# Kernel tuning notes

Measured on AMD Instinct MI355X. Metric: run time of the kernel, lower is better.

Reference implementation:

```python
import jax, jax.numpy as jnp
import numpy as np

BLOCK_SIZE = 32
QMAX = 31.0   # 6-bit symmetric: representable range [-32, 31], scale by absmax/31
QMIN = -32.0


def axs6_dequant(w: jnp.ndarray, block_size: int = BLOCK_SIZE) -> jnp.ndarray:
    """Block-wise 6-bit symmetric fake-quantization (quantize + dequantize)."""
    shape = w.shape
    wf = w.reshape(-1, block_size)                       # [n_blocks, block]
    scale = jnp.max(jnp.abs(wf), axis=1, keepdims=True) / QMAX
    scale = jnp.where(scale == 0, jnp.ones_like(scale), scale)
    q = jnp.clip(jnp.round(wf / scale), QMIN, QMAX)
    return (q * scale).reshape(shape)


def setup_inputs() -> dict:
    key = jax.random.key(0)
    k_x, k_w, k_b = jax.random.split(key, 3)
    C_in, C_out, K = 256, 512, 3
    x = jax.random.normal(k_x, (32, C_in, 56, 56), dtype=jnp.float32)
    # kaiming_uniform_(a=sqrt(5)) -> bound = sqrt(6 / ((1 + 5) * fan_in)) = 1/sqrt(fan_in)
    fan_in = C_in * K * K
    bound = 1.0 / np.sqrt(fan_in)
    weight = jax.random.uniform(k_w, (C_out, C_in, K, K), dtype=jnp.float32,
                                minval=-bound, maxval=bound)
    bias = jax.random.uniform(k_b, (C_out,), dtype=jnp.float32,
                              minval=-bound, maxval=bound)
    return {"x": x, "weight": weight, "bias": bias}


def reference(x, weight, bias):
    w_dq = axs6_dequant(weight, BLOCK_SIZE)
    out = jax.lax.conv_general_dilated(
        x, w_dq,
        window_strides=(1, 1),
        padding=((1, 1), (1, 1)),
        rhs_dilation=(1, 1),
        feature_group_count=1,
        dimension_numbers=("NCHW", "OIHW", "NCHW"),
    )
    return out + bias[None, :, None, None]
```

## Files before the change

kernel.cpp:

```cpp
#include <hip/hip_runtime.h>
#include <hip/hip_bf16.h>

typedef __bf16 bf16_t;
typedef __attribute__((ext_vector_type(8))) __bf16 bf16x8;
typedef __attribute__((ext_vector_type(4))) float f32x4;
typedef __attribute__((ext_vector_type(4))) int   i32x4;

#define C_IN   256
#define C_OUT  512
#define HW     3136
#define NB     32
#define HP     58
#define NQBLK  36864

#define NT   36
#define NWG  896

typedef const __attribute__((address_space(1))) unsigned int gu32;
typedef __attribute__((address_space(3))) unsigned int lu32;
__device__ __forceinline__ void gl16(const void* g, void* l) {
    __builtin_amdgcn_global_load_lds((gu32*)g, (lu32*)l, 16, 0, 0);
}
#define BAR()    __builtin_amdgcn_s_barrier()
#define PRIO(x)  __builtin_amdgcn_s_setprio(x)
#define SCHED0() __builtin_amdgcn_sched_barrier(0)

__device__ __forceinline__ bf16x8 asbf(i32x4 v) {
    union { i32x4 a; bf16x8 b; } u; u.a = v; return u.b;
}
__device__ __forceinline__ f32x4 MF(i32x4 a, i32x4 b, f32x4 c) {
    return __builtin_amdgcn_mfma_f32_16x16x32_bf16(asbf(a), asbf(b), c, 0, 0, 0);
}

__global__ void k_dequant(const float* __restrict__ w, bf16_t* __restrict__ wt) {
    int b = blockIdx.x * blockDim.x + threadIdx.x;
    if (b >= NQBLK) return;
    const float* src = w + (size_t)b * 32;
    float v[32];
    float amax = 0.f;
    #pragma unroll
    for (int i = 0; i < 32; i += 4) {
        float4 t = *reinterpret_cast<const float4*>(src + i);
        v[i] = t.x; v[i+1] = t.y; v[i+2] = t.z; v[i+3] = t.w;
        amax = fmaxf(amax, fmaxf(fmaxf(fabsf(t.x), fabsf(t.y)),
                                 fmaxf(fabsf(t.z), fabsf(t.w))));
    }
    float scale = amax / 31.0f;
    if (scale == 0.f) scale = 1.f;
    #pragma unroll
    for (int i = 0; i < 32; i++) {
        float q = rintf(v[i] / scale);
        q = fminf(31.f, fmaxf(-32.f, q));
        float dq = q * scale;
        int flat = b * 32 + i;
        int p    = flat % 9;
        int rest = flat / 9;
        int ci   = rest & 255;
        int co   = rest >> 8;
        wt[((size_t)(p * C_OUT + co) << 8) + ci] = (bf16_t)dq;
    }
}

__global__ void k_halo_zero(bf16_t* __restrict__ xT) {
    int idx = blockIdx.x * 256 + threadIdx.x;
    if (idx >= NB * 228 * 32) return;
    int c8 = idx & 31;
    int t  = idx >> 5;
    int p  = t % 228;
    int n  = t / 228;
    int hh, ww;
    if      (p < 58)  { hh = 0;           ww = p; }
    else if (p < 116) { hh = 57;          ww = p - 58; }
    else if (p < 172) { hh = p - 116 + 1; ww = 0; }
    else              { hh = p - 172 + 1; ww = 57; }
    size_t e = (((size_t)n * HP + hh) * HP + ww) * C_IN + c8 * 8;
    *reinterpret_cast<uint4*>(xT + e) = make_uint4(0, 0, 0, 0);
}

__global__ void k_x_nhwc(const float* __restrict__ x, bf16_t* __restrict__ xT) {
    __shared__ float tile[64][65];
    const int n   = blockIdx.z;
    const int cb  = blockIdx.y * 64;
    const int hwb = blockIdx.x * 64;
    const int t   = threadIdx.x;

    const int col = t & 63;
    const int r0  = t >> 6;
    #pragma unroll
    for (int k = 0; k < 16; k++) {
        int r = r0 * 16 + k;
        tile[r][col] = x[((size_t)(n * C_IN + cb + r)) * HW + hwb + col];
    }
    __syncthreads();

    const int j  = t >> 2;
    const int co = (t & 3) * 16;
    const int hw = hwb + j;
    const int hh = hw / 56, ww = hw - hh * 56;
    __align__(16) bf16_t vals[16];
    #pragma unroll
    for (int k = 0; k < 16; k++)
        vals[k] = (bf16_t)tile[co + k][j];
    bf16_t* dst = xT + (((size_t)n * HP + hh + 1) * HP + (ww + 1)) * C_IN + cb + co;
    *reinterpret_cast<uint4*>(dst)     = *reinterpret_cast<uint4*>(&vals[0]);
    *reinterpret_cast<uint4*>(dst + 8) = *reinterpret_cast<uint4*>(&vals[8]);
}

__global__ __launch_bounds__(512, 2) void k_conv_gemm(
    const bf16_t* __restrict__ xT, const bf16_t* __restrict__ wt,
    const float* __restrict__ bias, float* __restrict__ out)
{
    __shared__ __align__(16) bf16_t As[3][256][64];
    __shared__ __align__(16) bf16_t Bs[2][224][64];

    const int tid  = threadIdx.x;
    const int lane = tid & 63;
    const int wid  = tid >> 6;
    const int wr   = wid >> 1;
    const int wc   = wid & 1;

    const int orig  = blockIdx.x;
    const int wgid  = (orig & 7) * 112 + (orig >> 3);
    const int co0   = (wgid & 1) * 256;
    const int sband = wgid >> 1;
    const int nimg  = sband / 14;
    const int R0    = (sband - nimg * 14) * 4;

    const int trow = tid >> 3;
    const int lcx  = (tid & 7) ^ (trow & 7);

    const bf16_t* pA[4];
    const bf16_t* pB[4];
    #pragma unroll
    for (int i = 0; i < 4; i++) {
        pA[i] = wt + ((size_t)(co0 + i * 64 + trow) << 8) + lcx * 8;
        int r  = i * 64 + trow;
        int br = r / 56, bc = r - br * 56;
        pB[i] = xT + (((size_t)nimg * HP + R0 + br + 1) * HP + (bc + 1)) * C_IN + lcx * 8;
    }

    auto stageA2 = [&](int slot, int tk, int part) {
        const size_t off = ((size_t)(tk >> 2) << 17) + ((tk & 3) << 6);
        bf16_t* dst = &As[slot][0][0] + wid * 512;
        if (part == 0) { gl16(pA[0] + off, dst);        gl16(pA[1] + off, dst + 4096); }
        else           { gl16(pA[2] + off, dst + 8192); gl16(pA[3] + off, dst + 12288); }
    };
    auto stageB2 = [&](int buf, int tk, int part) {
        const int p  = tk >> 2;
        const int q3 = p / 3;
        const int off = ((q3 - 1) * HP + (p - q3 * 3) - 1) * C_IN + ((tk & 3) << 6);
        bf16_t* dst = &Bs[buf][0][0] + wid * 512;
        if (part == 0) { gl16(pB[0] + off, dst);        gl16(pB[1] + off, dst + 4096); }
        else           { gl16(pB[2] + off, dst + 8192);
                         if (tid < 256) gl16(pB[3] + off, dst + 12288); }
    };

    const int rl = lane & 15;
    const int kg = lane >> 4;
    const unsigned asBase = (unsigned)(uintptr_t)&As[0][0][0];
    const unsigned bsBase = (unsigned)(uintptr_t)&Bs[0][0][0];
    const unsigned aAddr0 = asBase + (unsigned)((wr * 64 + rl) * 128 + ((kg       ^ (rl & 7)) * 16));
    const unsigned aAddr1 = asBase + (unsigned)((wr * 64 + rl) * 128 + (((4 + kg) ^ (rl & 7)) * 16));
    const unsigned bAddr0 = bsBase + (unsigned)((wc * 112 + rl) * 128 + ((kg       ^ (rl & 7)) * 16));
    const unsigned bAddr1 = bsBase + (unsigned)((wc * 112 + rl) * 128 + (((4 + kg) ^ (rl & 7)) * 16));

    f32x4 acc[4][7];
    #pragma unroll
    for (int m = 0; m < 4; m++)
        #pragma unroll
        for (int j = 0; j < 7; j++)
            acc[m][j] = f32x4{0.f, 0.f, 0.f, 0.f};

    stageB2(0, 0, 0); stageB2(0, 0, 1);
    stageA2(0, 0, 0); stageA2(0, 0, 1);
    stageA2(1, 1, 0); stageA2(1, 1, 1);
    asm volatile("s_waitcnt vmcnt(4)" ::: "memory");
    BAR();
    SCHED0();

    i32x4 A00, A01, A10, A11, A20, A21, A30, A31;
    i32x4 S00, S01, S10, S11, S20, S21;
    int sr = 0;

#define ISSUE_B(D0, D1, OFFS) \
    asm volatile("ds_read_b128 %0, %2 offset:" OFFS "\n\t" \
                 "ds_read_b128 %1, %3 offset:" OFFS \
                 : "=v"(D0), "=v"(D1) : "v"(bT0), "v"(bT1));
#define LGKM(N) asm volatile("s_waitcnt lgkmcnt(" N ")" ::: "memory"); SCHED0();
#define MFMA8(J, X0, X1) \
    PRIO(1); \
    acc[0][J] = MF(A00, X0, acc[0][J]); acc[0][J] = MF(A01, X1, acc[0][J]); \
    acc[1][J] = MF(A10, X0, acc[1][J]); acc[1][J] = MF(A11, X1, acc[1][J]); \
    acc[2][J] = MF(A20, X0, acc[2][J]); acc[2][J] = MF(A21, X1, acc[2][J]); \
    acc[3][J] = MF(A30, X0, acc[3][J]); acc[3][J] = MF(A31, X1, acc[3][J]); \
    PRIO(0);

    #pragma unroll 1
    for (int t = 0; t < NT; ++t) {
        const unsigned aT0 = aAddr0 + (unsigned)sr * 32768u;
        const unsigned aT1 = aAddr1 + (unsigned)sr * 32768u;
        const unsigned bT0 = bAddr0 + (unsigned)(t & 1) * 28672u;
        const unsigned bT1 = bAddr1 + (unsigned)(t & 1) * 28672u;
        const int bnext = (t + 1) & 1;
        const int snext = sr + 2 >= 3 ? sr - 1 : sr + 2;

        asm volatile(
            "ds_read_b128 %0, %8 offset:0\n\t"
            "ds_read_b128 %1, %9 offset:0\n\t"
            "ds_read_b128 %2, %8 offset:2048\n\t"
            "ds_read_b128 %3, %9 offset:2048\n\t"
            "ds_read_b128 %4, %8 offset:4096\n\t"
            "ds_read_b128 %5, %9 offset:4096\n\t"
            "ds_read_b128 %6, %8 offset:6144\n\t"
            "ds_read_b128 %7, %9 offset:6144"
            : "=v"(A00), "=v"(A01), "=v"(A10), "=v"(A11),
              "=v"(A20), "=v"(A21), "=v"(A30), "=v"(A31)
            : "v"(aT0), "v"(aT1));
        ISSUE_B(S00, S01, "0");
        ISSUE_B(S10, S11, "2048");

        ISSUE_B(S20, S21, "4096");
        if (t + 1 < NT) stageB2(bnext, t + 1, 0);
        LGKM("4");
        MFMA8(0, S00, S01);

        ISSUE_B(S00, S01, "6144");
        if (t + 1 < NT) stageB2(bnext, t + 1, 1);
        LGKM("4");
        MFMA8(1, S10, S11);

        ISSUE_B(S10, S11, "8192");
        LGKM("4");
        MFMA8(2, S20, S21);

        ISSUE_B(S20, S21, "10240");
        if (t + 2 < NT) stageA2(snext, t + 2, 0);
        LGKM("4");
        MFMA8(3, S00, S01);

        ISSUE_B(S00, S01, "12288");
        LGKM("4");
        MFMA8(4, S10, S11);

        if (t + 2 < NT) stageA2(snext, t + 2, 1);
        LGKM("2");
        MFMA8(5, S20, S21);

        LGKM("0");
        MFMA8(6, S00, S01);

        if (t + 2 < NT)
            asm volatile("s_waitcnt vmcnt(4)" ::: "memory");
        else
            asm volatile("s_waitcnt vmcnt(0)" ::: "memory");
        BAR();
        SCHED0();
        sr = (sr + 1 >= 3) ? 0 : sr + 1;
    }
#undef ISSUE_B
#undef LGKM
#undef MFMA8

    int hw_off[7];
    #pragma unroll
    for (int j = 0; j < 7; j++) {
        int nn = wc * 112 + j * 16 + rl;
        int br = nn / 56, bc = nn - br * 56;
        hw_off[j] = (R0 + br) * 56 + bc;
    }
    const size_t obase = (size_t)nimg * C_OUT * HW;
    #pragma unroll
    for (int m = 0; m < 4; m++) {
        int cob = co0 + wr * 64 + m * 16 + ((lane >> 4) << 2);
        #pragma unroll
        for (int i = 0; i < 4; i++) {
            int co = cob + i;
            float bv = bias[co];
            float* orow = out + obase + (size_t)co * HW;
            #pragma unroll
            for (int j = 0; j < 7; j++)
                orow[hw_off[j]] = acc[m][j][i] + bv;
        }
    }
}

extern "C" void kernel_launch(void* const* d_in, const int* in_sizes, int n_in,
                              void* d_out, int out_size, void* d_ws, size_t ws_size,
                              hipStream_t stream) {
    const float* x    = (const float*)d_in[0];
    const float* w    = (const float*)d_in[1];
    const float* bias = (const float*)d_in[2];
    float* out = (float*)d_out;

    bf16_t* xT = (bf16_t*)d_ws;
    bf16_t* wt = (bf16_t*)((char*)d_ws + (size_t)NB * HP * HP * C_IN * 2);

    k_halo_zero<<<dim3((NB * 228 * 32 + 255) / 256), dim3(256), 0, stream>>>(xT);
    k_x_nhwc<<<dim3(49, 4, NB), dim3(256), 0, stream>>>(x, xT);
    k_dequant<<<dim3((NQBLK + 255) / 256), dim3(256), 0, stream>>>(w, wt);
    k_conv_gemm<<<dim3(NWG), dim3(512), 0, stream>>>(xT, wt, bias, out);
}
```

Baseline: 276.1 us.

## Double-buffer A fragments in registers and prefetch next tile's A during MFMAs

The K loop is unrolled by two, and the A operand fragments are now ping-ponged between two register sets. The next tile's A LDS reads are interleaved with the current tile's MFMA groups, so they no longer stall at the top of each iteration. The order of the global-to-LDS stages is changed, and the end-of-tile wait is tightened to vmcnt(0), which may cut the global-load overlap across tiles. The extra fragment registers raise VGPR pressure.

```diff
diff --git a/kernel.cpp b/kernel.cpp
--- a/kernel.cpp
+++ b/kernel.cpp
@@ -171,95 +171,89 @@
         for (int j = 0; j < 7; j++)
             acc[m][j] = f32x4{0.f, 0.f, 0.f, 0.f};
 
-    stageB2(0, 0, 0); stageB2(0, 0, 1);
+#define RD2(D0, D1, A0, A1, OFFS) \
+    asm volatile("ds_read_b128 %0, %2 offset:" OFFS "\n\t" \
+                 "ds_read_b128 %1, %3 offset:" OFFS \
+                 : "=v"(D0), "=v"(D1) : "v"(A0), "v"(A1));
+#define LGKM(N) asm volatile("s_waitcnt lgkmcnt(" N ")" ::: "memory"); SCHED0();
+#define MFMA8(AA, J, X0, X1) \
+    PRIO(1); \
+    acc[0][J] = MF(AA##00, X0, acc[0][J]); acc[0][J] = MF(AA##01, X1, acc[0][J]); \
+    acc[1][J] = MF(AA##10, X0, acc[1][J]); acc[1][J] = MF(AA##11, X1, acc[1][J]); \
+    acc[2][J] = MF(AA##20, X0, acc[2][J]); acc[2][J] = MF(AA##21, X1, acc[2][J]); \
+    acc[3][J] = MF(AA##30, X0, acc[3][J]); acc[3][J] = MF(AA##31, X1, acc[3][J]); \
+    PRIO(0);
+
+#define TILE(AC, AN, T, SR1, SR2, BCUR) do {                                  \
+    const unsigned bT0 = bAddr0 + (unsigned)(BCUR) * 28672u;                  \
+    const unsigned bT1 = bAddr1 + (unsigned)(BCUR) * 28672u;                  \
+    const unsigned nT0 = aAddr0 + (unsigned)(SR1) * 32768u;                   \
+    const unsigned nT1 = aAddr1 + (unsigned)(SR1) * 32768u;                   \
+    RD2(S00, S01, bT0, bT1, "0");                                             \
+    RD2(S10, S11, bT0, bT1, "2048");                                          \
+                                                                      \
+    RD2(S20, S21, bT0, bT1, "4096");                                          \
+    if ((T) + 2 < NT) stageA2((SR2), (T) + 2, 0);                             \
+    LGKM("4");  MFMA8(AC, 0, S00, S01);                                       \
+                                                                      \
+    RD2(S00, S01, bT0, bT1, "6144");                                          \
+    RD2(AN##00, AN##01, nT0, nT1, "0");                                       \
+    if ((T) + 2 < NT) stageA2((SR2), (T) + 2, 1);                             \
+    LGKM("6");  MFMA8(AC, 1, S10, S11);                                       \
+                                                                      \
+    RD2(S10, S11, bT0, bT1, "8192");                                          \
+    RD2(AN##10, AN##11, nT0, nT1, "2048");                                    \
+    if ((T) + 1 < NT) stageB2(((T) + 1) & 1, (T) + 1, 0);                     \
+    LGKM("8");  MFMA8(AC, 2, S20, S21);                                       \
+                                                                      \
+    RD2(S20, S21, bT0, bT1, "10240");                                         \
+    RD2(AN##20, AN##21, nT0, nT1, "4096");                                    \
+    if ((T) + 1 < NT) stageB2(((T) + 1) & 1, (T) + 1, 1);                     \
+    LGKM("10"); MFMA8(AC, 3, S00, S01);                                       \
+                                                                      \
+    RD2(S00, S01, bT0, bT1, "12288");                                         \
+    RD2(AN##30, AN##31, nT0, nT1, "6144");                                    \
+    LGKM("10"); MFMA8(AC, 4, S10, S11);                                       \
+                                                                      \
+    LGKM("6");  MFMA8(AC, 5, S20, S21);                                       \
+                                                                      \
+    LGKM("2");  MFMA8(AC, 6, S00, S01);                                       \
+    asm volatile("s_waitcnt vmcnt(0)" ::: "memory");                          \
+    BAR();                                                                    \
+    SCHED0();                                                                 \
+} while (0)
+
+    i32x4 Ea00, Ea01, Ea10, Ea11, Ea20, Ea21, Ea30, Ea31;
+    i32x4 Eb00, Eb01, Eb10, Eb11, Eb20, Eb21, Eb30, Eb31;
+    i32x4 S00, S01, S10, S11, S20, S21;
+
     stageA2(0, 0, 0); stageA2(0, 0, 1);
     stageA2(1, 1, 0); stageA2(1, 1, 1);
-    asm volatile("s_waitcnt vmcnt(4)" ::: "memory");
+    stageB2(0, 0, 0); stageB2(0, 0, 1);
+    asm volatile("s_waitcnt vmcnt(0)" ::: "memory");
     BAR();
     SCHED0();
-
-    i32x4 A00, A01, A10, A11, A20, A21, A30, A31;
-    i32x4 S00, S01, S10, S11, S20, S21;
+    RD2(Ea00, Ea01, aAddr0, aAddr1, "0");
+    RD2(Ea10, Ea11, aAddr0, aAddr1, "2048");
+    RD2(Ea20, Ea21, aAddr0, aAddr1, "4096");
+    RD2(Ea30, Ea31, aAddr0, aAddr1, "6144");
+
     int sr = 0;
-
-#define ISSUE_B(D0, D1, OFFS) \
-    asm volatile("ds_read_b128 %0, %2 offset:" OFFS "\n\t" \
-                 "ds_read_b128 %1, %3 offset:" OFFS \
-                 : "=v"(D0), "=v"(D1) : "v"(bT0), "v"(bT1));
-#define LGKM(N) asm volatile("s_waitcnt lgkmcnt(" N ")" ::: "memory"); SCHED0();
-#define MFMA8(J, X0, X1) \
-    PRIO(1); \
-    acc[0][J] = MF(A00, X0, acc[0][J]); acc[0][J] = MF(A01, X1, acc[0][J]); \
-    acc[1][J] = MF(A10, X0, acc[1][J]); acc[1][J] = MF(A11, X1, acc[1][J]); \
-    acc[2][J] = MF(A20, X0, acc[2][J]); acc[2][J] = MF(A21, X1, acc[2][J]); \
-    acc[3][J] = MF(A30, X0, acc[3][J]); acc[3][J] = MF(A31, X1, acc[3][J]); \
-    PRIO(0);
-
     #pragma unroll 1
-    for (int t = 0; t < NT; ++t) {
-        const unsigned aT0 = aAddr0 + (unsigned)sr * 32768u;
-        const unsigned aT1 = aAddr1 + (unsigned)sr * 32768u;
-        const unsigned bT0 = bAddr0 + (unsigned)(t & 1) * 28672u;
-        const unsigned bT1 = bAddr1 + (unsigned)(t & 1) * 28672u;
-        const int bnext = (t + 1) & 1;
-        const int snext = sr + 2 >= 3 ? sr - 1 : sr + 2;
-
-        asm volatile(
-            "ds_read_b128 %0, %8 offset:0\n\t"
-            "ds_read_b128 %1, %9 offset:0\n\t"
-            "ds_read_b128 %2, %8 offset:2048\n\t"
-            "ds_read_b128 %3, %9 offset:2048\n\t"
-            "ds_read_b128 %4, %8 offset:4096\n\t"
-            "ds_read_b128 %5, %9 offset:4096\n\t"
-            "ds_read_b128 %6, %8 offset:6144\n\t"
-            "ds_read_b128 %7, %9 offset:6144"
-            : "=v"(A00), "=v"(A01), "=v"(A10), "=v"(A11),
-              "=v"(A20), "=v"(A21), "=v"(A30), "=v"(A31)
-            : "v"(aT0), "v"(aT1));
-        ISSUE_B(S00, S01, "0");
-        ISSUE_B(S10, S11, "2048");
-
-        ISSUE_B(S20, S21, "4096");
-        if (t + 1 < NT) stageB2(bnext, t + 1, 0);
-        LGKM("4");
-        MFMA8(0, S00, S01);
-
-        ISSUE_B(S00, S01, "6144");
-        if (t + 1 < NT) stageB2(bnext, t + 1, 1);
-        LGKM("4");
-        MFMA8(1, S10, S11);
-
-        ISSUE_B(S10, S11, "8192");
-        LGKM("4");
-        MFMA8(2, S20, S21);
-
-        ISSUE_B(S20, S21, "10240");
-        if (t + 2 < NT) stageA2(snext, t + 2, 0);
-        LGKM("4");
-        MFMA8(3, S00, S01);
-
-        ISSUE_B(S00, S01, "12288");
-        LGKM("4");
-        MFMA8(4, S10, S11);
-
-        if (t + 2 < NT) stageA2(snext, t + 2, 1);
-        LGKM("2");
-        MFMA8(5, S20, S21);
-
-        LGKM("0");
-        MFMA8(6, S00, S01);
-
-        if (t + 2 < NT)
-            asm volatile("s_waitcnt vmcnt(4)" ::: "memory");
-        else
-            asm volatile("s_waitcnt vmcnt(0)" ::: "memory");
-        BAR();
-        SCHED0();
-        sr = (sr + 1 >= 3) ? 0 : sr + 1;
-    }
-#undef ISSUE_B
+    for (int t = 0; t < NT; t += 2) {
+        const int sr1 = (sr + 1 >= 3) ? sr - 2 : sr + 1;
+        const int sr2 = (sr + 2 >= 3) ? sr - 1 : sr + 2;
+        TILE(Ea, Eb, t,     sr1, sr2, 0);
+        TILE(Eb, Ea, t + 1, sr2, sr,  1);
+        sr = sr2;
+    }
+    asm volatile("s_waitcnt lgkmcnt(0)" ::: "memory");
+    SCHED0();
+
+#undef RD2
 #undef LGKM
 #undef MFMA8
+#undef TILE
 
     int hw_off[7];
     #pragma unroll
```

New measurement: 260.7 us. 1.06x faster.
